# Kernel optimization log

Hardware: AMD Instinct MI355X
Metric: run time of the kernel (lower is better)

The kernel has to match this reference:

```python
import jax, jax.numpy as jnp
import numpy as np

K = 16  # hard-coded neighborhood size
EPS = 1e-5


def knn_idx(coor_k, coor_q, k):
    # coor_*: (B, 3, N). Returns idx (B, Nq, k) of k nearest points in coor_k for each query.
    inner = jnp.einsum('bcn,bcm->bnm', coor_q, coor_k)
    sq_q = jnp.sum(coor_q ** 2, axis=1)  # (B, Nq)
    sq_k = jnp.sum(coor_k ** 2, axis=1)  # (B, Nk)
    dist = sq_q[:, :, None] + sq_k[:, None, :] - 2.0 * inner  # (B, Nq, Nk)
    return jax.lax.top_k(-dist, k)[1]


def fps(coor, num_group):
    # furthest point sampling, matching pointnet2 (start at index 0, squared dists).
    B, _, N = coor.shape
    xyz = jnp.transpose(coor, (0, 2, 1))  # (B, N, 3)

    def step(carry, _):
        dist, last = carry
        centroid = jnp.take_along_axis(xyz, last[:, None, None], axis=1)  # (B,1,3)
        d = jnp.sum((xyz - centroid) ** 2, axis=-1)  # (B, N)
        dist = jnp.minimum(dist, d)
        nxt = jnp.argmax(dist, axis=1).astype(jnp.int32)
        return (dist, nxt), last

    init = (jnp.full((B, N), 1e10, dtype=coor.dtype), jnp.zeros((B,), jnp.int32))
    _, idxs = jax.lax.scan(step, init, None, length=num_group)
    return jnp.transpose(idxs, (1, 0))  # (B, num_group)


def gather_points(x, idx):
    # x: (B, C, N), idx: (B, S) -> (B, C, S)
    return jnp.take_along_axis(x, idx[:, None, :], axis=2)


def get_graph_feature(coor_q, x_q, coor_k, x_k):
    # coor: (B,3,N), x: (B,C,N) -> (B, 2C, Nq, K)
    B, C, Nq = x_q.shape
    idx = jax.lax.stop_gradient(knn_idx(coor_k, coor_q, K))  # (B, Nq, K)
    idx_flat = jnp.broadcast_to(idx.reshape(B, 1, Nq * K), (B, C, Nq * K))
    nbr = jnp.take_along_axis(x_k, idx_flat, axis=2).reshape(B, C, Nq, K)
    xq = x_q[..., None]  # (B, C, Nq, 1)
    return jnp.concatenate([nbr - xq, jnp.broadcast_to(xq, nbr.shape)], axis=1)


def group_norm(x, gamma, beta, groups):
    # x: (B, C, N, K); normalize over (C//G, N, K) per sample per group.
    B, C = x.shape[0], x.shape[1]
    xr = x.reshape(B, groups, C // groups, *x.shape[2:])
    red = tuple(range(2, xr.ndim))
    mean = jnp.mean(xr, axis=red, keepdims=True)
    var = jnp.mean((xr - mean) ** 2, axis=red, keepdims=True)
    xn = ((xr - mean) * jax.lax.rsqrt(var + EPS)).reshape(x.shape)
    shp = (1, C) + (1,) * (x.ndim - 2)
    return xn * gamma.reshape(shp) + beta.reshape(shp)


def lrelu(x):
    return jnp.where(x >= 0, x, 0.2 * x)


def edge_layer(f, w, g, b):
    # 1x1 conv (no bias) + GroupNorm(4) + LeakyReLU(0.2)
    f = jnp.einsum('oc,bcnk->bonk', w, f)
    return lrelu(group_norm(f, g, b, 4))


def setup_inputs() -> dict:
    key = jax.random.key(0)
    ks = jax.random.split(key, 16)
    B, N = 32, 2048
    p = {}
    p['x'] = jax.random.normal(ks[0], (B, 3, N), dtype=jnp.float32)
    p['w_in'] = jax.random.normal(ks[1], (8, 3), dtype=jnp.float32) * 0.3
    p['b_in'] = jax.random.normal(ks[2], (8,), dtype=jnp.float32) * 0.1
    dims = [(32, 16), (64, 64), (64, 128), (128, 128)]
    for i, (o, c) in enumerate(dims, start=1):
        kw, kg, kb = jax.random.split(ks[2 + i], 3)
        p[f'w{i}'] = jax.random.normal(kw, (o, c), dtype=jnp.float32) * (1.0 / np.sqrt(c))
        p[f'g{i}'] = 1.0 + 0.1 * jax.random.normal(kg, (o,), dtype=jnp.float32)
        p[f'b{i}'] = 0.1 * jax.random.normal(kb, (o,), dtype=jnp.float32)
    return p


def reference(x, w_in, b_in, w1, g1, b1, w2, g2, b2, w3, g3, b3, w4, g4, b4):
    coor = x
    f = jnp.einsum('oc,bcn->bon', w_in, x) + b_in[None, :, None]  # (B,8,N)

    f = get_graph_feature(coor, f, coor, f)          # (B,16,N,K)
    f = jnp.max(edge_layer(f, w1, g1, b1), axis=-1)  # (B,32,N)

    idx = jax.lax.stop_gradient(fps(coor, 512))
    coor_q, f_q = gather_points(coor, idx), gather_points(f, idx)
    f = get_graph_feature(coor_q, f_q, coor, f)      # (B,64,512,K)
    f = jnp.max(edge_layer(f, w2, g2, b2), axis=-1)  # (B,64,512)
    coor = coor_q

    f = get_graph_feature(coor, f, coor, f)          # (B,128,512,K)
    f = jnp.max(edge_layer(f, w3, g3, b3), axis=-1)  # (B,64,512)

    idx = jax.lax.stop_gradient(fps(coor, 128))
    coor_q, f_q = gather_points(coor, idx), gather_points(f, idx)
    f = get_graph_feature(coor_q, f_q, coor, f)      # (B,128,128,K)
    f = jnp.max(edge_layer(f, w4, g4, b4), axis=-1)  # (B,128,128)
    coor = coor_q
    return coor, f
```

## Files before the change

### kernel.cpp

```cpp
#include <hip/hip_runtime.h>
#include <hip/hip_bf16.h>

#define DEV __device__ __forceinline__

DEV float bf2f(unsigned short u){ return __uint_as_float(((unsigned)u)<<16); }
DEV unsigned short f2bf(float f){
  unsigned u = __float_as_uint(f);
  u += 0x7fffu + ((u>>16)&1u);
  return (unsigned short)(u>>16);
}

template<int CTRL>
DEV unsigned long long dpp_umax(unsigned long long k){
  int lo = (int)(unsigned)k;
  int hi = (int)(unsigned)(k>>32);
  int plo = __builtin_amdgcn_update_dpp(lo, lo, CTRL, 0xF, 0xF, false);
  int phi = __builtin_amdgcn_update_dpp(hi, hi, CTRL, 0xF, 0xF, false);
  unsigned long long p = ((unsigned long long)(unsigned)phi << 32) | (unsigned)plo;
  return (p > k) ? p : k;
}

__global__ __launch_bounds__(256) void detect_kernel(
    const unsigned short* __restrict__ x, int* __restrict__ flag){
  __shared__ int cnt;
  if (threadIdx.x==0) cnt = 0;
  __syncthreads();
  int local = 0;
  for (int i=threadIdx.x; i<4096; i+=256){
    int e = (x[i]>>7)&0xFF;
    if (e >= 0xC0) local++;
  }
  atomicAdd(&cnt, local);
  __syncthreads();
  if (threadIdx.x==0) *flag = (cnt > 64) ? 1 : 0;
}

struct PConv {
  const void* s[14];
  float*      d[14];
  int         sz[14];
};

__global__ __launch_bounds__(256) void prep_kernel(
    const void* __restrict__ xraw, const int* __restrict__ flag,
    const void* __restrict__ w_in_raw, const void* __restrict__ b_in_raw,
    PConv p,
    float* __restrict__ xyz0, float* __restrict__ f0, float* __restrict__ stats){
  bool isf = (*flag != 0);
  int bx = blockIdx.x;
  if (bx < 117){
    int i = bx*256 + threadIdx.x;
    int seg = 0, off = i;
    #pragma unroll
    for (seg=0; seg<14; ++seg){
      if (off < p.sz[seg]) break;
      off -= p.sz[seg];
    }
    if (seg >= 14) return;
    float v = isf ? ((const float*)p.s[seg])[off]
                  : bf2f(((const unsigned short*)p.s[seg])[off]);
    p.d[seg][off] = v;
    return;
  }
  int i = (bx-117)*256 + threadIdx.x;
  if (i < 8192) stats[i] = 0.f;
  int b = i >> 11, n = i & 2047;
  size_t base = (size_t)b*3*2048 + n;
  float X, Y, Z;
  if (isf){
    const float* xf = (const float*)xraw;
    X = xf[base]; Y = xf[base+2048]; Z = xf[base+4096];
  } else {
    const unsigned short* xu = (const unsigned short*)xraw;
    X = bf2f(xu[base]); Y = bf2f(xu[base+2048]); Z = bf2f(xu[base+4096]);
  }
  float* o3 = xyz0 + (size_t)i*3;
  o3[0]=X; o3[1]=Y; o3[2]=Z;
  const float* wf = (const float*)w_in_raw;
  const float* bf = (const float*)b_in_raw;
  const unsigned short* wu = (const unsigned short*)w_in_raw;
  const unsigned short* bu = (const unsigned short*)b_in_raw;
  float* fo = f0 + (size_t)i*8;
  #pragma unroll
  for (int o=0;o<8;++o){
    float w0 = isf ? wf[o*3+0] : bf2f(wu[o*3+0]);
    float w1 = isf ? wf[o*3+1] : bf2f(wu[o*3+1]);
    float w2 = isf ? wf[o*3+2] : bf2f(wu[o*3+2]);
    float bb = isf ? bf[o]     : bf2f(bu[o]);
    fo[o] = w0*X + w1*Y + w2*Z + bb;
  }
}

template<int NK, int QB>
DEV void knn_body(float* smem, const float* __restrict__ qxyz,
                  const float* __restrict__ kxyz, int Nq,
                  int* __restrict__ oidx, int bx, int b){
  float4* kd = (float4*)smem;
  int t = threadIdx.x;
  for (int i=t; i<NK; i+=256){
    const float* p = kxyz + ((size_t)b*NK + i)*3;
    float X=p[0], Y=p[1], Z=p[2];
    float sk = __fadd_rn(__fadd_rn(__fmul_rn(X,X),__fmul_rn(Y,Y)),__fmul_rn(Z,Z));
    kd[i] = make_float4(X,Y,Z,sk);
  }
  __syncthreads();
  int ql = t>>2, h = t&3;
  int q0 = bx*QB;
  const float* qp = qxyz + ((size_t)b*Nq + q0 + ql)*3;
  float QX=qp[0], QY=qp[1], QZ=qp[2];
  float sq = __fadd_rn(__fadd_rn(__fmul_rn(QX,QX),__fmul_rn(QY,QY)),__fmul_rn(QZ,QZ));
  float dl[16]; int il[16];
  #pragma unroll
  for (int j=0;j<16;++j){ dl[j]=3.4e38f; il[j]=-1; }
  for (int i=0; i<NK/4; i+=8){
    float d[8];
    #pragma unroll
    for (int u=0;u<8;++u){
      float4 c = kd[4*(i+u)+h];
      float dot = __fadd_rn(__fadd_rn(__fmul_rn(QX,c.x),__fmul_rn(QY,c.y)),__fmul_rn(QZ,c.z));
      d[u] = __fsub_rn(__fadd_rn(sq, c.w), __fmul_rn(2.0f,dot));
    }
    float dmin = fminf(fminf(fminf(d[0],d[1]),fminf(d[2],d[3])),
                       fminf(fminf(d[4],d[5]),fminf(d[6],d[7])));
    if (dmin < dl[15]){
      #pragma unroll
      for (int u=0;u<8;++u){
        float du = d[u];
        if (du < dl[15]){
          dl[15]=du; il[15]=4*(i+u)+h;
          #pragma unroll
          for (int s=15;s>0;--s){
            if (dl[s] < dl[s-1]){
              float td=dl[s]; dl[s]=dl[s-1]; dl[s-1]=td;
              int   ti=il[s]; il[s]=il[s-1]; il[s-1]=ti;
            }
          }
        }
      }
    }
  }
  __syncthreads();
  float* dbuf = smem;
  int*   ibuf = (int*)(smem + QB*65);
  int base = ql*65 + h*16;
  #pragma unroll
  for (int j=0;j<16;++j){ dbuf[base+j]=dl[j]; ibuf[base+j]=il[j]; }
  __syncthreads();
  if (t < QB){
    const float* db = dbuf + t*65;
    const int*   ib = ibuf + t*65;
    int p0=0,p1=0,p2=0,p3=0;
    int* op = oidx + ((size_t)b*Nq + q0 + t)*16;
    #pragma unroll 1
    for (int j=0;j<16;++j){
      float e0 = (p0<16)? db[p0]    : 3.5e38f; int i0 = (p0<16)? ib[p0]    : 0x7fffffff;
      float e1 = (p1<16)? db[16+p1] : 3.5e38f; int i1 = (p1<16)? ib[16+p1] : 0x7fffffff;
      float e2 = (p2<16)? db[32+p2] : 3.5e38f; int i2 = (p2<16)? ib[32+p2] : 0x7fffffff;
      float e3 = (p3<16)? db[48+p3] : 3.5e38f; int i3 = (p3<16)? ib[48+p3] : 0x7fffffff;
      float bd=e0; int bi=i0; int bh=0;
      if (e1<bd || (e1==bd && i1<bi)){ bd=e1; bi=i1; bh=1; }
      if (e2<bd || (e2==bd && i2<bi)){ bd=e2; bi=i2; bh=2; }
      if (e3<bd || (e3==bd && i3<bi)){ bd=e3; bi=i3; bh=3; }
      op[j]=bi;
      p0 += (bh==0); p1 += (bh==1); p2 += (bh==2); p3 += (bh==3);
    }
  }
  __syncthreads();
}

template<int NP,int G>
DEV void fps_body(float* smem, const float* __restrict__ xyz,
                  int* __restrict__ oidx, float* __restrict__ oxyz, int b){
  constexpr int PPT = NP/256;
  __builtin_amdgcn_s_setprio(3);
  float4* xl4 = (float4*)smem;
  unsigned long long* candK = (unsigned long long*)(smem + NP*4);
  float4* candX = (float4*)(smem + NP*4 + 16);
  int* selidx = (int*)(smem + NP*4 + 48);
  int t = threadIdx.x, w = t>>6;
  float px[PPT], py[PPT], pz[PPT], dist[PPT];
  #pragma unroll
  for (int j=0;j<PPT;++j){
    int gi = t + j*256;
    const float* p = xyz + ((size_t)b*NP + gi)*3;
    float X=p[0], Y=p[1], Z=p[2];
    px[j]=X; py[j]=Y; pz[j]=Z; dist[j]=1e10f;
    xl4[gi] = make_float4(X,Y,Z,0.f);
  }
  if (t==0) selidx[0] = 0;
  __syncthreads();
  float4 c0 = xl4[0];
  float cx=c0.x, cy=c0.y, cz=c0.z;
  int Bi = 0;
  for (int g=1; g<G; ++g){
    float bv=-1.f; int bi=0; float bxc=0.f, byc=0.f, bzc=0.f;
    #pragma unroll
    for (int j=0;j<PPT;++j){
      float dx=__fsub_rn(px[j],cx), dy=__fsub_rn(py[j],cy), dz=__fsub_rn(pz[j],cz);
      float d = __fadd_rn(__fadd_rn(__fmul_rn(dx,dx),__fmul_rn(dy,dy)),__fmul_rn(dz,dz));
      float nd = fminf(dist[j], d);
      dist[j] = nd;
      bool cc = (nd > bv);
      bv = cc ? nd : bv;
      bi = cc ? (t + j*256) : bi;
      bxc = cc ? px[j] : bxc; byc = cc ? py[j] : byc; bzc = cc ? pz[j] : bzc;
    }
    unsigned long long klocal =
        ((unsigned long long)__float_as_uint(bv) << 32) | (unsigned)(0xFFFFFFFFu - bi);
    unsigned long long k = klocal;
    k = dpp_umax<0x111>(k);
    k = dpp_umax<0x112>(k);
    k = dpp_umax<0x114>(k);
    k = dpp_umax<0x118>(k);
    k = dpp_umax<0x142>(k);
    k = dpp_umax<0x143>(k);
    unsigned klo = (unsigned)__builtin_amdgcn_readlane((int)(unsigned)k, 63);
    unsigned khi = (unsigned)__builtin_amdgcn_readlane((int)(unsigned)(k>>32), 63);
    unsigned long long wkey = ((unsigned long long)khi<<32) | klo;
    int par = g & 1;
    if (klocal == wkey){
      candK[par*4 + w] = wkey;
      candX[par*4 + w] = make_float4(bxc, byc, bzc, 0.f);
    }
    __syncthreads();
    unsigned long long kk = candK[par*4+0]; float4 xx = candX[par*4+0];
    unsigned long long k1 = candK[par*4+1]; float4 x1 = candX[par*4+1];
    if (k1 > kk){ kk=k1; xx=x1; }
    unsigned long long k2 = candK[par*4+2]; float4 x2 = candX[par*4+2];
    if (k2 > kk){ kk=k2; xx=x2; }
    unsigned long long k3 = candK[par*4+3]; float4 x3 = candX[par*4+3];
    if (k3 > kk){ kk=k3; xx=x3; }
    Bi = (int)(0xFFFFFFFFu - (unsigned)kk);
    cx = xx.x; cy = xx.y; cz = xx.z;
    if (t==0) selidx[g] = Bi;
  }
  __syncthreads();
  for (int i=t; i<G; i+=256){
    int s = selidx[i];
    float4 c = xl4[s];
    oidx[(size_t)b*G + i] = s;
    float* op = oxyz + ((size_t)b*G + i)*3;
    op[0]=c.x; op[1]=c.y; op[2]=c.z;
  }
}

template<int CF,int COUT,int QB>
DEV void edge_body(float* smem, const float* __restrict__ fk,
                   const int* __restrict__ sel, const int* __restrict__ knn,
                   const float* __restrict__ w, float* __restrict__ mm,
                   float* __restrict__ stats, int Nq, int Nk, int bx, int b){
  constexpr int CIN = 2*CF;
  constexpr int GPQ = COUT/2;
  constexpr int WS  = COUT+1;
  constexpr int ESTR= CF*16+8;
  constexpr int WTB = ((CF*WS+3)&~3);
  static_assert(QB*GPQ == 256, "block mapping");
  float* wtb = smem;
  float* e   = smem + WTB;
  float* fqs = e + QB*ESTR;
  float* sS  = fqs + QB*CF;
  int t = threadIdx.x;
  int q0 = bx*QB;

  if (t<8) sS[t]=0.f;
  for (int i=t; i<QB*CF; i+=256){
    int ql = i/CF, c = i&(CF-1);
    int qi = sel ? sel[b*Nq + q0 + ql] : (q0 + ql);
    fqs[i] = fk[((size_t)b*Nk + qi)*CF + c];
  }
  for (int i=t; i<CF*COUT; i+=256){
    int o = i/CF, c = i&(CF-1);
    wtb[c*WS+o] = w[o*CIN + c];
  }
  if (t < QB*16){
    int ql = t>>4, k = t&15;
    int nid = knn[((size_t)b*Nq + q0 + ql)*16 + k];
    const float4* row = (const float4*)(fk + ((size_t)b*Nk + nid)*CF);
    float* ep = e + ql*ESTR + k;
    #pragma unroll
    for (int c4=0; c4<CF/4; ++c4){
      float4 v = row[c4];
      ep[(c4*4+0)*16]=v.x; ep[(c4*4+1)*16]=v.y; ep[(c4*4+2)*16]=v.z; ep[(c4*4+3)*16]=v.w;
    }
  }
  __syncthreads();

  int ql = t/GPQ, o = t%GPQ;
  const float* eb = e + ql*ESTR;
  const float* fqb = fqs + ql*CF;
  float y0[16], y1[16];
  #pragma unroll
  for (int k=0;k<16;++k){ y0[k]=0.f; y1[k]=0.f; }
  float zA0=0.f, zA1=0.f;
  for (int c=0;c<CF;++c){
    float w0 = wtb[c*WS+o];
    float w1 = wtb[c*WS+o+GPQ];
    float fqc = fqb[c];
    zA0 = fmaf(w0,fqc,zA0); zA1 = fmaf(w1,fqc,zA1);
    const float4* ev4 = (const float4*)(eb + c*16);
    #pragma unroll
    for (int k4=0;k4<4;++k4){
      float4 ev = ev4[k4];
      y0[k4*4+0]=fmaf(w0,ev.x,y0[k4*4+0]); y0[k4*4+1]=fmaf(w0,ev.y,y0[k4*4+1]);
      y0[k4*4+2]=fmaf(w0,ev.z,y0[k4*4+2]); y0[k4*4+3]=fmaf(w0,ev.w,y0[k4*4+3]);
      y1[k4*4+0]=fmaf(w1,ev.x,y1[k4*4+0]); y1[k4*4+1]=fmaf(w1,ev.y,y1[k4*4+1]);
      y1[k4*4+2]=fmaf(w1,ev.z,y1[k4*4+2]); y1[k4*4+3]=fmaf(w1,ev.w,y1[k4*4+3]);
    }
  }
  __syncthreads();
  for (int i=t; i<CF*COUT; i+=256){
    int oo = i/CF, c = i&(CF-1);
    wtb[c*WS+oo] = w[oo*CIN + CF + c];
  }
  __syncthreads();
  float zB0=0.f, zB1=0.f;
  for (int c=0;c<CF;++c){
    float fqc = fqb[c];
    zB0 = fmaf(wtb[c*WS+o],fqc,zB0);
    zB1 = fmaf(wtb[c*WS+o+GPQ],fqc,zB1);
  }
  float z0 = zB0 - zA0, z1 = zB1 - zA1;

  float mx0=-3.4e38f, mn0=3.4e38f, s0=0.f, q0s=0.f;
  float mx1=-3.4e38f, mn1=3.4e38f, s1=0.f, q1s=0.f;
  #pragma unroll
  for (int k=0;k<16;++k){
    float v0 = y0[k]+z0, v1 = y1[k]+z1;
    mx0=fmaxf(mx0,v0); mn0=fminf(mn0,v0); s0+=v0; q0s=fmaf(v0,v0,q0s);
    mx1=fmaxf(mx1,v1); mn1=fminf(mn1,v1); s1+=v1; q1s=fmaf(v1,v1,q1s);
  }
  int g0 = o/(COUT/4);
  atomicAdd(&sS[g0],   s0); atomicAdd(&sS[4+g0],   q0s);
  atomicAdd(&sS[g0+2], s1); atomicAdd(&sS[6+g0],   q1s);
  size_t mi0 = ((size_t)b*Nq + q0 + ql)*COUT + o;
  ((float2*)mm)[mi0]       = make_float2(mx0,mn0);
  ((float2*)mm)[mi0+GPQ]   = make_float2(mx1,mn1);
  __syncthreads();
  if (t<8){
    int g = t>>1, which = t&1;
    float val = which ? sS[4+g] : sS[g];
    atomicAdd(&stats[(((size_t)b*4+g)*8 + (bx&7))*2 + which], val);
  }
}

__global__ __launch_bounds__(256,4) void fused1_kernel(
    const float* __restrict__ xyz0, int* __restrict__ knnb1,
    int* __restrict__ idx1, float* __restrict__ xyz1){
  __shared__ __align__(16) float smem[8752];
  int bx = blockIdx.x;
  if (bx < 32){
    fps_body<2048,512>(smem, xyz0, idx1, xyz1, bx);
  } else {
    int rid = bx - 32;
    knn_body<2048,64>(smem, xyz0, xyz0, 2048, knnb1, rid & 31, rid >> 5);
  }
}

__global__ __launch_bounds__(256,4) void fused2_kernel(
    const float* __restrict__ xyz0, const float* __restrict__ xyz1,
    const int* __restrict__ knnb1,
    int* __restrict__ knnb2, int* __restrict__ knnb3,
    int* __restrict__ idx2, float* __restrict__ xyz2,
    const float* __restrict__ f0, const float* __restrict__ cw1,
    float* __restrict__ mmb, float* __restrict__ stats1){
  __shared__ __align__(16) float smem[8320];
  int bx = blockIdx.x;
  if (bx < 32){
    fps_body<512,128>(smem, xyz1, idx2, xyz2, bx);
  } else if (bx < 288){
    int rid = bx - 32;
    knn_body<2048,64>(smem, xyz1, xyz0, 512, knnb2, rid & 7, rid >> 3);
  } else if (bx < 544){
    int rid = bx - 288;
    knn_body<512,64>(smem, xyz1, xyz1, 512, knnb3, rid & 7, rid >> 3);
  } else {
    int rid = bx - 544;
    edge_body<8,32,16>(smem, f0, nullptr, knnb1, cw1, mmb, stats1,
                       2048, 2048, rid & 127, rid >> 7);
  }
}

__global__ __launch_bounds__(256,4) void fused3_kernel(
    const float* __restrict__ xyz1, const float* __restrict__ xyz2,
    int* __restrict__ knnb4,
    const float* __restrict__ f1, const int* __restrict__ idx1,
    const int* __restrict__ knnb2, const float* __restrict__ cw2,
    float* __restrict__ mmb, float* __restrict__ stats2){
  __shared__ __align__(16) float smem[8320];
  int bx = blockIdx.x;
  if (bx < 64){
    knn_body<512,64>(smem, xyz2, xyz1, 128, knnb4, bx & 1, bx >> 1);
  } else {
    int rid = bx - 64;
    edge_body<32,64,8>(smem, f1, idx1, knnb2, cw2, mmb, stats2,
                       512, 2048, rid & 63, rid >> 6);
  }
}

template<int CF,int COUT,int QB>
__global__ __launch_bounds__(256) void edge_kernel(
    const float* __restrict__ fk, const int* __restrict__ sel,
    const int* __restrict__ knn, const float* __restrict__ w,
    float* __restrict__ mm, float* __restrict__ stats, int Nq, int Nk){
  constexpr int WS  = COUT+1;
  constexpr int ESTR= CF*16+8;
  constexpr int WTB = ((CF*WS+3)&~3);
  constexpr int SM  = WTB + QB*ESTR + QB*CF + 8;
  __shared__ __align__(16) float smem[SM];
  edge_body<CF,COUT,QB>(smem, fk, sel, knn, w, mm, stats, Nq, Nk,
                        blockIdx.x, blockIdx.y);
}

__global__ __launch_bounds__(256) void fin_kernel(
    const float* __restrict__ mm, const float* __restrict__ stats,
    const float* __restrict__ gam, const float* __restrict__ bet,
    float* __restrict__ fo, void* __restrict__ outbase, const int* __restrict__ flag,
    int outoff, int Nq, int COUT, float invcnt, int total){
  for (int i = blockIdx.x*256 + threadIdx.x; i<total; i += gridDim.x*256){
    int o = i % COUT;
    int r = i / COUT;
    int q = r % Nq;
    int b = r / Nq;
    int g = o / (COUT>>2);
    const float* sp = stats + ((size_t)(b*4+g))*16;
    float s=0.f, s2=0.f;
    #pragma unroll
    for (int nb=0;nb<8;++nb){ s += sp[nb*2]; s2 += sp[nb*2+1]; }
    float mean = s*invcnt;
    float var  = fmaxf(s2*invcnt - mean*mean, 0.f);
    float inv  = 1.0f / sqrtf(var + 1e-5f);
    float a  = gam[o] * inv;
    float bb = bet[o] - a*mean;
    const float* mp = mm + (size_t)i*2;
    float xv = (a>=0.f) ? mp[0] : mp[1];
    float v = fmaf(a, xv, bb);
    v = (v>=0.f) ? v : 0.2f*v;
    if (fo) fo[i]=v;
    if (outbase){
      int idx = outoff + ((b*COUT + o)*Nq + q);
      if (*flag) ((float*)outbase)[idx] = v;
      else       ((unsigned short*)outbase)[idx] = f2bf(v);
    }
  }
}

__global__ __launch_bounds__(256) void coor_kernel(
    const float* __restrict__ xyz2, void* __restrict__ outbase,
    const int* __restrict__ flag){
  int i = blockIdx.x*256+threadIdx.x;
  int m = i & 127;
  int c = (i>>7) % 3;
  int b = i / 384;
  float v = xyz2[((size_t)b*128+m)*3 + c];
  if (*flag) ((float*)outbase)[i] = v;
  else       ((unsigned short*)outbase)[i] = f2bf(v);
}

extern "C" void kernel_launch(void* const* d_in, const int* in_sizes, int n_in,
                              void* d_out, int out_size, void* d_ws, size_t ws_size,
                              hipStream_t stream){
  float* W    = (float*)d_ws;
  float* xyz0 = W;
  float* f0   = W + 196608;
  float* f1   = W + 720896;
  float* xyz1 = W + 2818048;
  float* f2   = W + 2867200;
  float* f3   = W + 3915776;
  float* xyz2 = W + 4964352;
  float* stats= W + 4976640;
  int*   flag = (int*)(W + 4984832);
  float* PRM  = W + 4984848;
  int*  idx1  = (int*)(W + 5014640);
  int*  idx2  = (int*)(W + 5031024);
  float* SCR  = W + 5035120;
  int*   knnb = (int*)SCR;
  int*   knnb4= (int*)SCR;
  int*   knnb2= (int*)f3;
  int*   knnb3= (int*)f3 + 262144;
  float* mmb  = SCR + 1048576;

  float* cw_in = PRM;
  float* cb_in = PRM+24;
  float* cw1 = PRM+32;   float* cg1 = PRM+544;   float* cbb1 = PRM+576;
  float* cw2 = PRM+608;  float* cg2 = PRM+4704;  float* cbb2 = PRM+4768;
  float* cw3 = PRM+4832; float* cg3 = PRM+13024; float* cbb3 = PRM+13088;
  float* cw4 = PRM+13152;float* cg4 = PRM+29536; float* cbb4 = PRM+29664;

  detect_kernel<<<1,256,0,stream>>>((const unsigned short*)d_in[0], flag);

  PConv pc;
  const int psz[14] = {24,8,512,32,32,4096,64,64,8192,64,64,16384,128,128};
  float* pdst[14] = {cw_in,cb_in,cw1,cg1,cbb1,cw2,cg2,cbb2,cw3,cg3,cbb3,cw4,cg4,cbb4};
  for (int j=0;j<14;++j){ pc.s[j]=d_in[j+1]; pc.d[j]=pdst[j]; pc.sz[j]=psz[j]; }

  prep_kernel<<<373,256,0,stream>>>(d_in[0], flag, d_in[1], d_in[2], pc,
                                    xyz0, f0, stats);

  fused1_kernel<<<1056,256,0,stream>>>(xyz0, knnb, idx1, xyz1);

  fused2_kernel<<<4640,256,0,stream>>>(xyz0, xyz1, knnb, knnb2, knnb3,
                                       idx2, xyz2, f0, cw1, mmb, stats+0);

  coor_kernel<<<48,256,0,stream>>>(xyz2, d_out, flag);

  fin_kernel<<<1024,256,0,stream>>>(mmb, stats+0, cg1, cbb1, f1, nullptr, flag, 0, 2048, 32, 1.f/262144.f, 2097152);

  fused3_kernel<<<2112,256,0,stream>>>(xyz1, xyz2, knnb4,
                                       f1, idx1, knnb2, cw2, mmb, stats+2048);
  fin_kernel<<<1024,256,0,stream>>>(mmb, stats+2048, cg2, cbb2, f2, nullptr, flag, 0, 512, 64, 1.f/131072.f, 1048576);

  edge_kernel<64,64,8><<<dim3(64,32),256,0,stream>>>(f2, nullptr, knnb3, cw3, mmb, stats+4096, 512, 512);
  fin_kernel<<<1024,256,0,stream>>>(mmb, stats+4096, cg3, cbb3, f3, nullptr, flag, 0, 512, 64, 1.f/131072.f, 1048576);

  edge_kernel<64,128,4><<<dim3(32,32),256,0,stream>>>(f3, idx2, knnb4, cw4, mmb, stats+6144, 128, 512);
  fin_kernel<<<1024,256,0,stream>>>(mmb, stats+6144, cg4, cbb4, nullptr, d_out, flag, 12288, 128, 128, 1.f/65536.f, 524288);
}
```

Measured before the change: 762.8 us.

## Use bitonic packed-key top-k in kNN and fold small kernels into neighbors

The kNN inner loop now packs each distance and index into a sortable 64-bit key. It sorts batches of 8 with a bitonic network and merges them into a 16-entry list with a branch-free merge, replacing the data-dependent insertion sort. The final 4-way merge works on packed keys. The detect kernel is folded into prep_kernel, with every block recomputing the flag, and the coor kernel is folded into fused3 as extra blocks, which removes two launches. The branch-free merge does more compare-exchange work per batch than the early-out path, and 64-bit keys increase register pressure.

```diff
diff --git a/kernel.cpp b/kernel.cpp
--- a/kernel.cpp
+++ b/kernel.cpp
@@ -2,6 +2,7 @@
 #include <hip/hip_bf16.h>
 
 #define DEV __device__ __forceinline__
+typedef unsigned long long u64;
 
 DEV float bf2f(unsigned short u){ return __uint_as_float(((unsigned)u)<<16); }
 DEV unsigned short f2bf(float f){
@@ -11,28 +12,49 @@
 }
 
 template<int CTRL>
-DEV unsigned long long dpp_umax(unsigned long long k){
+DEV u64 dpp_umax(u64 k){
   int lo = (int)(unsigned)k;
   int hi = (int)(unsigned)(k>>32);
   int plo = __builtin_amdgcn_update_dpp(lo, lo, CTRL, 0xF, 0xF, false);
   int phi = __builtin_amdgcn_update_dpp(hi, hi, CTRL, 0xF, 0xF, false);
-  unsigned long long p = ((unsigned long long)(unsigned)phi << 32) | (unsigned)plo;
+  u64 p = ((u64)(unsigned)phi << 32) | (unsigned)plo;
   return (p > k) ? p : k;
 }
 
-__global__ __launch_bounds__(256) void detect_kernel(
-    const unsigned short* __restrict__ x, int* __restrict__ flag){
-  __shared__ int cnt;
-  if (threadIdx.x==0) cnt = 0;
-  __syncthreads();
-  int local = 0;
-  for (int i=threadIdx.x; i<4096; i+=256){
-    int e = (x[i]>>7)&0xFF;
-    if (e >= 0xC0) local++;
-  }
-  atomicAdd(&cnt, local);
-  __syncthreads();
-  if (threadIdx.x==0) *flag = (cnt > 64) ? 1 : 0;
+DEV void ce64(u64 &a, u64 &b){
+  u64 lo = (a<b)?a:b;
+  u64 hi = (a<b)?b:a;
+  a = lo; b = hi;
+}
+DEV void sort8(u64* x){
+  #pragma unroll
+  for (int k=2;k<=8;k<<=1){
+    #pragma unroll
+    for (int j=k>>1;j>0;j>>=1){
+      #pragma unroll
+      for (int i=0;i<8;++i){
+        int l = i^j;
+        if (l>i){
+          if ((i&k)==0) ce64(x[i],x[l]);
+          else          ce64(x[l],x[i]);
+        }
+      }
+    }
+  }
+}
+DEV void bm16(u64* A){
+  #pragma unroll
+  for (int gap=8;gap>0;gap>>=1){
+    #pragma unroll
+    for (int i=0;i<16;++i){
+      if ((i&gap)==0) ce64(A[i], A[i|gap]);
+    }
+  }
+}
+DEV unsigned f2sort(float d){
+  unsigned ub = __float_as_uint(d);
+  unsigned s  = (unsigned)((int)ub >> 31);
+  return ub ^ (s | 0x80000000u);
 }
 
 struct PConv {
@@ -42,14 +64,29 @@
 };
 
 __global__ __launch_bounds__(256) void prep_kernel(
-    const void* __restrict__ xraw, const int* __restrict__ flag,
+    const void* __restrict__ xraw, int* __restrict__ flagw,
     const void* __restrict__ w_in_raw, const void* __restrict__ b_in_raw,
     PConv p,
     float* __restrict__ xyz0, float* __restrict__ f0, float* __restrict__ stats){
-  bool isf = (*flag != 0);
+  __shared__ int cnt;
+  int t = threadIdx.x;
+  if (t==0) cnt = 0;
+  __syncthreads();
+  {
+    const unsigned short* xs = (const unsigned short*)xraw;
+    int local = 0;
+    for (int i=t; i<4096; i+=256){
+      int e = (xs[i]>>7)&0xFF;
+      if (e >= 0xC0) local++;
+    }
+    atomicAdd(&cnt, local);
+  }
+  __syncthreads();
+  bool isf = (cnt > 64);
   int bx = blockIdx.x;
+  if (bx==0 && t==0) *flagw = isf ? 1 : 0;
   if (bx < 117){
-    int i = bx*256 + threadIdx.x;
+    int i = bx*256 + t;
     int seg = 0, off = i;
     #pragma unroll
     for (seg=0; seg<14; ++seg){
@@ -62,7 +99,7 @@
     p.d[seg][off] = v;
     return;
   }
-  int i = (bx-117)*256 + threadIdx.x;
+  int i = (bx-117)*256 + t;
   if (i < 8192) stats[i] = 0.f;
   int b = i >> 11, n = i & 2047;
   size_t base = (size_t)b*3*2048 + n;
@@ -96,6 +133,7 @@
                   const float* __restrict__ kxyz, int Nq,
                   int* __restrict__ oidx, int bx, int b){
   float4* kd = (float4*)smem;
+  u64* lbuf  = (u64*)smem;
   int t = threadIdx.x;
   for (int i=t; i<NK; i+=256){
     const float* p = kxyz + ((size_t)b*NK + i)*3;
@@ -109,60 +147,50 @@
   const float* qp = qxyz + ((size_t)b*Nq + q0 + ql)*3;
   float QX=qp[0], QY=qp[1], QZ=qp[2];
   float sq = __fadd_rn(__fadd_rn(__fmul_rn(QX,QX),__fmul_rn(QY,QY)),__fmul_rn(QZ,QZ));
-  float dl[16]; int il[16];
-  #pragma unroll
-  for (int j=0;j<16;++j){ dl[j]=3.4e38f; il[j]=-1; }
+  u64 A[16];
+  #pragma unroll
+  for (int j=0;j<16;++j) A[j] = ~0ULL;
+  #pragma unroll 1
   for (int i=0; i<NK/4; i+=8){
-    float d[8];
+    u64 k8[8];
     #pragma unroll
     for (int u=0;u<8;++u){
-      float4 c = kd[4*(i+u)+h];
+      int cidx = 4*(i+u)+h;
+      float4 c = kd[cidx];
       float dot = __fadd_rn(__fadd_rn(__fmul_rn(QX,c.x),__fmul_rn(QY,c.y)),__fmul_rn(QZ,c.z));
-      d[u] = __fsub_rn(__fadd_rn(sq, c.w), __fmul_rn(2.0f,dot));
-    }
-    float dmin = fminf(fminf(fminf(d[0],d[1]),fminf(d[2],d[3])),
-                       fminf(fminf(d[4],d[5]),fminf(d[6],d[7])));
-    if (dmin < dl[15]){
-      #pragma unroll
-      for (int u=0;u<8;++u){
-        float du = d[u];
-        if (du < dl[15]){
-          dl[15]=du; il[15]=4*(i+u)+h;
-          #pragma unroll
-          for (int s=15;s>0;--s){
-            if (dl[s] < dl[s-1]){
-              float td=dl[s]; dl[s]=dl[s-1]; dl[s-1]=td;
-              int   ti=il[s]; il[s]=il[s-1]; il[s-1]=ti;
-            }
-          }
-        }
-      }
-    }
-  }
-  __syncthreads();
-  float* dbuf = smem;
-  int*   ibuf = (int*)(smem + QB*65);
-  int base = ql*65 + h*16;
-  #pragma unroll
-  for (int j=0;j<16;++j){ dbuf[base+j]=dl[j]; ibuf[base+j]=il[j]; }
+      float d = __fsub_rn(__fadd_rn(sq, c.w), __fmul_rn(2.0f,dot));
+      k8[u] = ((u64)f2sort(d)<<32) | (unsigned)cidx;
+    }
+    sort8(k8);
+    #pragma unroll
+    for (int s=0;s<8;++s){
+      u64 bb = k8[7-s];
+      u64 a  = A[8+s];
+      A[8+s] = (bb < a) ? bb : a;
+    }
+    bm16(A);
+  }
+  __syncthreads();
+  u64* Lq = lbuf + ((size_t)ql*65 + (size_t)h*16);
+  #pragma unroll
+  for (int j=0;j<16;++j) Lq[j] = A[j];
   __syncthreads();
   if (t < QB){
-    const float* db = dbuf + t*65;
-    const int*   ib = ibuf + t*65;
+    const u64* db = lbuf + (size_t)t*65;
     int p0=0,p1=0,p2=0,p3=0;
+    u64 e0=db[0], e1=db[16], e2=db[32], e3=db[48];
     int* op = oidx + ((size_t)b*Nq + q0 + t)*16;
     #pragma unroll 1
     for (int j=0;j<16;++j){
-      float e0 = (p0<16)? db[p0]    : 3.5e38f; int i0 = (p0<16)? ib[p0]    : 0x7fffffff;
-      float e1 = (p1<16)? db[16+p1] : 3.5e38f; int i1 = (p1<16)? ib[16+p1] : 0x7fffffff;
-      float e2 = (p2<16)? db[32+p2] : 3.5e38f; int i2 = (p2<16)? ib[32+p2] : 0x7fffffff;
-      float e3 = (p3<16)? db[48+p3] : 3.5e38f; int i3 = (p3<16)? ib[48+p3] : 0x7fffffff;
-      float bd=e0; int bi=i0; int bh=0;
-      if (e1<bd || (e1==bd && i1<bi)){ bd=e1; bi=i1; bh=1; }
-      if (e2<bd || (e2==bd && i2<bi)){ bd=e2; bi=i2; bh=2; }
-      if (e3<bd || (e3==bd && i3<bi)){ bd=e3; bi=i3; bh=3; }
-      op[j]=bi;
-      p0 += (bh==0); p1 += (bh==1); p2 += (bh==2); p3 += (bh==3);
+      u64 bd = e0; int bh = 0;
+      if (e1 < bd){ bd=e1; bh=1; }
+      if (e2 < bd){ bd=e2; bh=2; }
+      if (e3 < bd){ bd=e3; bh=3; }
+      op[j] = (int)(unsigned)bd;
+      if      (bh==0){ p0++; e0 = (p0<16)? db[p0]    : ~0ULL; }
+      else if (bh==1){ p1++; e1 = (p1<16)? db[16+p1] : ~0ULL; }
+      else if (bh==2){ p2++; e2 = (p2<16)? db[32+p2] : ~0ULL; }
+      else           { p3++; e3 = (p3<16)? db[48+p3] : ~0ULL; }
     }
   }
   __syncthreads();
@@ -174,7 +202,7 @@
   constexpr int PPT = NP/256;
   __builtin_amdgcn_s_setprio(3);
   float4* xl4 = (float4*)smem;
-  unsigned long long* candK = (unsigned long long*)(smem + NP*4);
+  u64* candK = (u64*)(smem + NP*4);
   float4* candX = (float4*)(smem + NP*4 + 16);
   int* selidx = (int*)(smem + NP*4 + 48);
   int t = threadIdx.x, w = t>>6;
@@ -205,9 +233,8 @@
       bi = cc ? (t + j*256) : bi;
       bxc = cc ? px[j] : bxc; byc = cc ? py[j] : byc; bzc = cc ? pz[j] : bzc;
     }
-    unsigned long long klocal =
-        ((unsigned long long)__float_as_uint(bv) << 32) | (unsigned)(0xFFFFFFFFu - bi);
-    unsigned long long k = klocal;
+    u64 klocal = ((u64)__float_as_uint(bv) << 32) | (unsigned)(0xFFFFFFFFu - bi);
+    u64 k = klocal;
     k = dpp_umax<0x111>(k);
     k = dpp_umax<0x112>(k);
     k = dpp_umax<0x114>(k);
@@ -216,19 +243,19 @@
     k = dpp_umax<0x143>(k);
     unsigned klo = (unsigned)__builtin_amdgcn_readlane((int)(unsigned)k, 63);
     unsigned khi = (unsigned)__builtin_amdgcn_readlane((int)(unsigned)(k>>32), 63);
-    unsigned long long wkey = ((unsigned long long)khi<<32) | klo;
+    u64 wkey = ((u64)khi<<32) | klo;
     int par = g & 1;
     if (klocal == wkey){
       candK[par*4 + w] = wkey;
       candX[par*4 + w] = make_float4(bxc, byc, bzc, 0.f);
     }
     __syncthreads();
-    unsigned long long kk = candK[par*4+0]; float4 xx = candX[par*4+0];
-    unsigned long long k1 = candK[par*4+1]; float4 x1 = candX[par*4+1];
+    u64 kk = candK[par*4+0]; float4 xx = candX[par*4+0];
+    u64 k1 = candK[par*4+1]; float4 x1 = candX[par*4+1];
     if (k1 > kk){ kk=k1; xx=x1; }
-    unsigned long long k2 = candK[par*4+2]; float4 x2 = candX[par*4+2];
+    u64 k2 = candK[par*4+2]; float4 x2 = candX[par*4+2];
     if (k2 > kk){ kk=k2; xx=x2; }
-    unsigned long long k3 = candK[par*4+3]; float4 x3 = candX[par*4+3];
+    u64 k3 = candK[par*4+3]; float4 x3 = candX[par*4+3];
     if (k3 > kk){ kk=k3; xx=x3; }
     Bi = (int)(0xFFFFFFFFu - (unsigned)kk);
     cx = xx.x; cy = xx.y; cz = xx.z;
@@ -341,6 +368,18 @@
     float val = which ? sS[4+g] : sS[g];
     atomicAdd(&stats[(((size_t)b*4+g)*8 + (bx&7))*2 + which], val);
   }
+}
+
+DEV void coor_body(const float* __restrict__ xyz2, void* __restrict__ outbase,
+                   const int* __restrict__ flag, int bx){
+  int i = bx*256 + threadIdx.x;
+  if (i >= 12288) return;
+  int m = i & 127;
+  int c = (i>>7) % 3;
+  int b = i / 384;
+  float v = xyz2[((size_t)b*128+m)*3 + c];
+  if (*flag) ((float*)outbase)[i] = v;
+  else       ((unsigned short*)outbase)[i] = f2bf(v);
 }
 
 __global__ __launch_bounds__(256,4) void fused1_kernel(
@@ -385,15 +424,18 @@
     int* __restrict__ knnb4,
     const float* __restrict__ f1, const int* __restrict__ idx1,
     const int* __restrict__ knnb2, const float* __restrict__ cw2,
-    float* __restrict__ mmb, float* __restrict__ stats2){
+    float* __restrict__ mmb, float* __restrict__ stats2,
+    void* __restrict__ outbase, const int* __restrict__ flag){
   __shared__ __align__(16) float smem[8320];
   int bx = blockIdx.x;
   if (bx < 64){
     knn_body<512,64>(smem, xyz2, xyz1, 128, knnb4, bx & 1, bx >> 1);
-  } else {
+  } else if (bx < 2112){
     int rid = bx - 64;
     edge_body<32,64,8>(smem, f1, idx1, knnb2, cw2, mmb, stats2,
                        512, 2048, rid & 63, rid >> 6);
+  } else {
+    coor_body(xyz2, outbase, flag, bx - 2112);
   }
 }
 
@@ -442,18 +484,6 @@
       else       ((unsigned short*)outbase)[idx] = f2bf(v);
     }
   }
-}
-
-__global__ __launch_bounds__(256) void coor_kernel(
-    const float* __restrict__ xyz2, void* __restrict__ outbase,
-    const int* __restrict__ flag){
-  int i = blockIdx.x*256+threadIdx.x;
-  int m = i & 127;
-  int c = (i>>7) % 3;
-  int b = i / 384;
-  float v = xyz2[((size_t)b*128+m)*3 + c];
-  if (*flag) ((float*)outbase)[i] = v;
-  else       ((unsigned short*)outbase)[i] = f2bf(v);
 }
 
 extern "C" void kernel_launch(void* const* d_in, const int* in_sizes, int n_in,
@@ -486,8 +516,6 @@
   float* cw3 = PRM+4832; float* cg3 = PRM+13024; float* cbb3 = PRM+13088;
   float* cw4 = PRM+13152;float* cg4 = PRM+29536; float* cbb4 = PRM+29664;
 
-  detect_kernel<<<1,256,0,stream>>>((const unsigned short*)d_in[0], flag);
-
   PConv pc;
   const int psz[14] = {24,8,512,32,32,4096,64,64,8192,64,64,16384,128,128};
   float* pdst[14] = {cw_in,cb_in,cw1,cg1,cbb1,cw2,cg2,cbb2,cw3,cg3,cbb3,cw4,cg4,cbb4};
@@ -501,12 +529,11 @@
   fused2_kernel<<<4640,256,0,stream>>>(xyz0, xyz1, knnb, knnb2, knnb3,
                                        idx2, xyz2, f0, cw1, mmb, stats+0);
 
-  coor_kernel<<<48,256,0,stream>>>(xyz2, d_out, flag);
-
   fin_kernel<<<1024,256,0,stream>>>(mmb, stats+0, cg1, cbb1, f1, nullptr, flag, 0, 2048, 32, 1.f/262144.f, 2097152);
 
-  fused3_kernel<<<2112,256,0,stream>>>(xyz1, xyz2, knnb4,
-                                       f1, idx1, knnb2, cw2, mmb, stats+2048);
+  fused3_kernel<<<2160,256,0,stream>>>(xyz1, xyz2, knnb4,
+                                       f1, idx1, knnb2, cw2, mmb, stats+2048,
+                                       d_out, flag);
   fin_kernel<<<1024,256,0,stream>>>(mmb, stats+2048, cg2, cbb2, f2, nullptr, flag, 0, 512, 64, 1.f/131072.f, 1048576);
 
   edge_kernel<64,64,8><<<dim3(64,32),256,0,stream>>>(f2, nullptr, knnb3, cw3, mmb, stats+4096, 512, 512);
```

After: 620.6 us, median of 2. 1.23x faster.
